# Kernel tuning notes

Hardware: AMD Instinct MI355X
Metric: run time of the kernel (lower is better)

Reference implementation:

```python
import jax, jax.numpy as jnp
import numpy as np

N_EX, N_KC, D, HID, NHEADS = 10000, 500, 128, 128, 2
B, S = 256, 500
ALPHA = 0.2
NEG = -9e15


def setup_inputs() -> dict:
    key = jax.random.key(0)
    ks = jax.random.split(key, 24)
    sc = 0.1
    inp = {
        "adj_exercise_kc": jax.random.randint(ks[0], (N_EX, N_KC), 0, 2, dtype=jnp.int32),
        "kc_data": jax.random.randint(ks[1], (B, S), 0, N_KC).astype(jnp.int64),
        "exercise_data": jax.random.randint(ks[2], (B, S), 0, N_EX + 1).astype(jnp.int64),
        "exercise_respond_data": jax.random.randint(ks[3], (B, S), 0, 2 * N_EX + 1).astype(jnp.int64),
        "target": jax.random.randint(ks[4], (B * (S - 1), 1), 0, 2).astype(jnp.float32),
        # learned parameters
        "ex_embed": jax.random.normal(ks[5], (N_EX, D)) * sc,
        "kc_embed": jax.random.normal(ks[6], (N_KC, D)) * sc,
        "W1": jax.random.normal(ks[7], (NHEADS, D, D)) * sc,        # per-head shared proj
        "a_att": jax.random.normal(ks[8], (NHEADS, 2 * D, 1)) * sc,  # attention vector
        "E": jax.random.normal(ks[9], (NHEADS, D, D)) * sc,
        "rd_w": jax.random.normal(ks[10], (NHEADS, D, 2 * D)) * sc,  # reduceDim (mode 3)
        "rd_b": jnp.zeros((NHEADS, D)),
        "w_ih": jax.random.normal(ks[11], (4 * HID, 2 * D)) * sc,
        "w_hh": jax.random.normal(ks[12], (4 * HID, HID)) * sc,
        "b_ih": jnp.zeros((4 * HID,)),
        "b_hh": jnp.zeros((4 * HID,)),
        "fc1_w": jax.random.normal(ks[13], (HID, D + HID)) * sc,
        "fc1_b": jnp.zeros((HID,)),
        "fc2_w": jax.random.normal(ks[14], (1, HID)) * sc,
        "fc2_b": jnp.zeros((1,)),
    }
    return inp


def _gat_head(ex_h, kc_h, adj, W1h, ah, Eh, rdw, rdb):
    # mode == 3 GAT head. a_input @ a decomposes: e[i,j] = LReLU(exWh[i].a1 + kcWh[j].a2)
    kc_Wh = kc_h @ W1h                                   # [Nkc, D]
    ex_Wh = ex_h @ W1h                                   # [Nex, D]
    e = jax.nn.leaky_relu(ex_Wh @ ah[:D] + (kc_Wh @ ah[D:]).T, ALPHA)  # [Nex, Nkc]
    att = jax.nn.softmax(jnp.where(adj > 0, e, NEG), axis=1)
    new_kc = att @ kc_Wh                                 # [Nex, D]
    ex_Eh = ex_h @ Eh
    emb = jnp.concatenate([new_kc, new_kc * ex_Eh], axis=1) @ rdw.T + rdb
    return jax.nn.elu(emb)                               # [Nex, D]


def _lstm(x, w_ih, w_hh, b_ih, b_hh):
    # single-layer torch LSTM, gate order i,f,g,o
    b = x.shape[0]
    xg = jnp.einsum('bsi,gi->sbg', x, w_ih) + b_ih + b_hh  # [S,B,4H]

    def step(carry, xt):
        h, c = carry
        g = xt + h @ w_hh.T
        i, f, gg, o = jnp.split(g, 4, axis=-1)
        c = jax.nn.sigmoid(f) * c + jax.nn.sigmoid(i) * jnp.tanh(gg)
        h = jax.nn.sigmoid(o) * jnp.tanh(c)
        return (h, c), h

    init = (jnp.zeros((b, HID), x.dtype), jnp.zeros((b, HID), x.dtype))
    _, hs = jax.lax.scan(step, init, xg)
    return jnp.swapaxes(hs, 0, 1)                        # [B,S,H]


def _forward(adj, exercise_data, respond_data, target,
             ex_embed, kc_embed, W1, a_att, E, rd_w, rd_b,
             w_ih, w_hh, b_ih, b_hh, fc1_w, fc1_b, fc2_w, fc2_b):
    heads = jax.vmap(_gat_head, in_axes=(None, None, None, 0, 0, 0, 0, 0))(
        ex_embed, kc_embed, adj, W1, a_att, E, rd_w, rd_b)   # [NH, Nex, D]
    # torch: cat(dim=1).view(Nex, D, NH).mean(2) -> interleaved reshape of the concat
    cat = jnp.swapaxes(heads, 0, 1).reshape(N_EX, NHEADS * D)
    exercise_embedding = cat.reshape(N_EX, D, NHEADS).mean(-1)  # [Nex, D]

    emb0 = jnp.concatenate([jnp.zeros((1, D), exercise_embedding.dtype), exercise_embedding], 0)
    assess = emb0[exercise_data]                          # [B,S,D]

    zeros = jnp.zeros_like(exercise_embedding)
    resp_emb = jnp.concatenate([
        jnp.concatenate([zeros, exercise_embedding], -1),
        jnp.concatenate([exercise_embedding, zeros], -1)], 0)  # [2Nex, 2D]
    resp0 = jnp.concatenate([jnp.zeros((1, 2 * D), resp_emb.dtype), resp_emb], 0)
    lstm_input = resp0[respond_data]                      # [B,S,2D]

    learn = _lstm(lstm_input, w_ih, w_hh, b_ih, b_hh)[:, :S - 1, :]  # [B,S-1,H]
    assess = assess[:, 1:, :]                             # [B,S-1,D]

    y = jax.nn.relu(jnp.concatenate([learn, assess], -1) @ fc1_w.T + fc1_b)
    pred = (y @ fc2_w.T + fc2_b).reshape(-1)              # [B*(S-1)]
    t = target.reshape(-1)                                # all targets >= 0 => mask all-true
    # BCE with logits, mean reduction
    loss = jnp.mean(jnp.maximum(pred, 0) - pred * t + jnp.log1p(jnp.exp(-jnp.abs(pred))))
    return loss, jax.nn.sigmoid(pred), t


def reference(adj_exercise_kc, kc_data, exercise_data, exercise_respond_data, target,
              ex_embed, kc_embed, W1, a_att, E, rd_w, rd_b,
              w_ih, w_hh, b_ih, b_hh, fc1_w, fc1_b, fc2_w, fc2_b):
    del kc_data  # unused by the original forward body
    return _forward(adj_exercise_kc, exercise_data, exercise_respond_data, target,
                    ex_embed, kc_embed, W1, a_att, E, rd_w, rd_b,
                    w_ih, w_hh, b_ih, b_hh, fc1_w, fc1_b, fc2_w, fc2_b)
```

## Files before the change

### kernel.cpp

```cpp
#include <hip/hip_runtime.h>
#include <math.h>

#define N_EX 10000
#define N_KC 500
#define D 128
#define HID 128
#define BB 256
#define SS 500
#define NROWS 127744

typedef float vf4 __attribute__((ext_vector_type(4)));
typedef _Float16 hf2 __attribute__((ext_vector_type(2)));
typedef _Float16 hf8 __attribute__((ext_vector_type(8)));
typedef float f32x4 __attribute__((ext_vector_type(4)));

__device__ __forceinline__ float sigm(float x) { return 1.f / (1.f + __expf(-x)); }
__device__ __forceinline__ float tanh_fast(float x) { return 1.f - 2.f / (1.f + __expf(2.f * x)); }

__device__ __forceinline__ hf2 u2h(unsigned v) { union { unsigned u; hf2 h; } x; x.u = v; return x.h; }

__device__ __forceinline__ float quad_sum(float x) {
    int a = __builtin_amdgcn_update_dpp(0, __float_as_int(x), 0xB1, 0xF, 0xF, true);
    x += __int_as_float(a);
    int b = __builtin_amdgcn_update_dpp(0, __float_as_int(x), 0x4E, 0xF, 0xF, true);
    x += __int_as_float(b);
    return x;
}

__global__ void k_precomp(const float* rd_w, const float* w_ih, const float* fc1_w,
                          const float* b_ih, const float* b_hh, const float* W1, const float* a_att,
                          const float* w_hh,
                          float* rd_wT, unsigned short* w_all16, unsigned short* fc1A16,
                          float* gb512, float* v1,
                          unsigned short* wlstm16, float* projC) {
    int idx = blockIdx.x * blockDim.x + threadIdx.x;
    int stride = gridDim.x * blockDim.x;
    const int N1 = 2 * 256 * 128;
    const int NW = 1152 * 128;
    const int NF = 128 * 128;
    const int NG = 512;
    const int N7 = 256;
    const int N8 = 65536;
    int total = N1 + NW + NF + NG + N7 + N8;
    for (int tt = idx; tt < total; tt += stride) {
        int u = tt;
        if (u < N1) {
            int h = u / (256 * 128); int rem = u % (256 * 128); int c = rem / 128; int dd = rem % 128;
            rd_wT[u] = rd_w[h * 128 * 256 + dd * 256 + c];
        } else if ((u -= N1) < NW) {
            int n = u >> 7, k = u & 127;
            float val;
            if (n < 512) {
                int c = n; val = w_ih[((c & 3) * 128 + (c >> 2)) * 256 + 128 + k];
            } else if (n < 1024) {
                int c = n - 512; val = w_ih[((c & 3) * 128 + (c >> 2)) * 256 + k];
            } else {
                int j = n - 1024; val = fc1_w[j * 256 + 128 + k];
            }
            ((_Float16*)w_all16)[u] = (_Float16)val;
        } else if ((u -= NW) < NF) {
            int j = u >> 7, k = u & 127;
            ((_Float16*)fc1A16)[u] = (_Float16)fc1_w[j * 256 + k];
        } else if ((u -= NF) < NG) {
            int c = u;
            float v = b_ih[(c & 3) * 128 + (c >> 2)] + b_hh[(c & 3) * 128 + (c >> 2)];
            gb512[c] = v;
            projC[c] = v;
        } else if ((u -= NG) < N7) {
            int h = u / 128, k = u % 128;
            const float* wr = W1 + h * 16384 + k * 128;
            const float* av = a_att + h * 256;
            float acc = 0.f;
            for (int d = 0; d < 128; ++d) acc += wr[d] * av[d];
            v1[u] = acc;
        } else {
            u -= N7;
            int x = u & 7;
            int t = (u >> 3) & 511;
            int i = u >> 12;
            int g = i >> 2, j = i & 3;
            int uu = t >> 2, q = t & 3;
            float val = w_hh[(g * 128 + uu) * 128 + q * 32 + j * 8 + x];
            ((_Float16*)wlstm16)[u] = (_Float16)val;
        }
    }
}

__global__ void k_kc(const float* kc_embed, const float* W1, const float* a_att,
                     float* kcWhT, float* s_kc) {
    int j = blockIdx.x, h = blockIdx.y, d = threadIdx.x;
    __shared__ float row[128];
    __shared__ float red[128];
    row[d] = kc_embed[j * 128 + d];
    __syncthreads();
    const float* w = W1 + h * 16384;
    float acc = 0.f;
    for (int k = 0; k < 128; ++k) acc += row[k] * w[k * 128 + d];
    kcWhT[((size_t)(h * 128 + d)) * 500 + j] = acc;
    red[d] = acc * a_att[h * 256 + 128 + d];
    __syncthreads();
    for (int s = 64; s > 0; s >>= 1) { if (d < s) red[d] += red[d + s]; __syncthreads(); }
    if (d == 0) s_kc[h * 500 + j] = red[0];
}

__global__ void k_sex(const float* ex_embed, const float* v1, float* s_ex) {
    int t = blockIdx.x * blockDim.x + threadIdx.x;
    if (t >= 2 * N_EX) return;
    int h = t / N_EX, i = t % N_EX;
    const float4* e4 = (const float4*)(ex_embed + (size_t)i * 128);
    const float4* v4 = (const float4*)(v1 + h * 128);
    float acc = 0.f;
    for (int k = 0; k < 32; ++k) {
        float4 a = e4[k], b = v4[k];
        acc += a.x * b.x + a.y * b.y + a.z * b.z + a.w * b.w;
    }
    s_ex[h * N_EX + i] = acc;
}

__global__ __launch_bounds__(256) void k_attnk(const int* adj, const float* s_ex, const float* s_kc,
                                               const float* kcWhT, float* new_kc) {
    int i0 = blockIdx.x * 8, t = threadIdx.x;
    __shared__ vf4 at4[2][1500];
    __shared__ float skc_l[2][500];
    float* at0 = (float*)at4[0];
    float* at1 = (float*)at4[1];
    for (int j = t; j < 1000; j += 256) ((float*)skc_l)[j] = s_kc[j];
    __syncthreads();
    {
        int lg = t >> 5, lane = t & 31;
        int i = i0 + lg;
        float sex0 = s_ex[i];
        float sex1 = s_ex[N_EX + i];
        const int* arow = adj + (size_t)i * 500;
        float lmax0 = -INFINITY, lmax1 = -INFINITY;
        for (int j = lane; j < 500; j += 32) {
            bool m = arow[j] > 0;
            float e0 = sex0 + skc_l[0][j];
            e0 = (e0 >= 0.f) ? e0 : 0.2f * e0;
            e0 = m ? e0 : -INFINITY;
            float e1 = sex1 + skc_l[1][j];
            e1 = (e1 >= 0.f) ? e1 : 0.2f * e1;
            e1 = m ? e1 : -INFINITY;
            at0[j * 12 + lg] = e0;
            at1[j * 12 + lg] = e1;
            lmax0 = fmaxf(lmax0, e0);
            lmax1 = fmaxf(lmax1, e1);
        }
#pragma unroll
        for (int m = 16; m > 0; m >>= 1) {
            lmax0 = fmaxf(lmax0, __shfl_xor(lmax0, m));
            lmax1 = fmaxf(lmax1, __shfl_xor(lmax1, m));
        }
        float lsum0 = 0.f, lsum1 = 0.f;
        for (int j = lane; j < 500; j += 32) {
            float w0 = __expf(at0[j * 12 + lg] - lmax0);
            float w1 = __expf(at1[j * 12 + lg] - lmax1);
            at0[j * 12 + lg] = w0;
            at1[j * 12 + lg] = w1;
            lsum0 += w0; lsum1 += w1;
        }
#pragma unroll
        for (int m = 16; m > 0; m >>= 1) {
            lsum0 += __shfl_xor(lsum0, m);
            lsum1 += __shfl_xor(lsum1, m);
        }
        float inv0 = 1.f / lsum0, inv1 = 1.f / lsum1;
        for (int j = lane; j < 500; j += 32) {
            at0[j * 12 + lg] *= inv0;
            at1[j * 12 + lg] *= inv1;
        }
    }
    __syncthreads();
    int d = t & 127, half = t >> 7;
    for (int h = 0; h < 2; ++h) {
        const float* at = (h == 0) ? at0 : at1;
        const float* kcwd = kcWhT + ((size_t)(h * 128 + d)) * 500;
        vf4 acc = {0.f, 0.f, 0.f, 0.f};
        for (int j4 = 0; j4 < 125; ++j4) {
            vf4 w = *(const vf4*)(kcwd + j4 * 4);
            vf4 a0 = *(const vf4*)(at + (j4 * 4 + 0) * 12 + half * 4);
            vf4 a1 = *(const vf4*)(at + (j4 * 4 + 1) * 12 + half * 4);
            vf4 a2 = *(const vf4*)(at + (j4 * 4 + 2) * 12 + half * 4);
            vf4 a3 = *(const vf4*)(at + (j4 * 4 + 3) * 12 + half * 4);
            acc += a0 * w.x + a1 * w.y + a2 * w.z + a3 * w.w;
        }
        new_kc[((size_t)h * N_EX + i0 + half * 4 + 0) * 128 + d] = acc.x;
        new_kc[((size_t)h * N_EX + i0 + half * 4 + 1) * 128 + d] = acc.y;
        new_kc[((size_t)h * N_EX + i0 + half * 4 + 2) * 128 + d] = acc.z;
        new_kc[((size_t)h * N_EX + i0 + half * 4 + 3) * 128 + d] = acc.w;
    }
}

__global__ __launch_bounds__(256) void k_gat2m(const float* new_kc, const float* ex_embed,
                                               const float* E, const float* rd_wT,
                                               const float* rd_b, _Float16* emb16) {
    int i0 = blockIdx.x * 8, t = threadIdx.x;
    int d = t & 127, half = t >> 7;
    __shared__ float exrT[128 * 8];
    __shared__ float nkT[2][128 * 8];
    __shared__ float prT[128 * 8];
    __shared__ float Hl[2][8 * 128];
    for (int idx = t; idx < 8 * 128; idx += 256) {
        int r = idx >> 7, k = idx & 127;
        exrT[k * 8 + r]   = ex_embed[(size_t)i0 * 128 + idx];
        nkT[0][k * 8 + r] = new_kc[((size_t)i0) * 128 + idx];
        nkT[1][k * 8 + r] = new_kc[((size_t)N_EX + i0) * 128 + idx];
    }
    __syncthreads();
    for (int h = 0; h < 2; ++h) {
        const float* Eh = E + h * 16384;
        const float* rt = rd_wT + h * 256 * 128;
        float rb = rd_b[h * 128 + d];
        vf4 acc2 = {0.f, 0.f, 0.f, 0.f};
        for (int k = 0; k < 128; ++k) {
            float ev = Eh[k * 128 + d];
            vf4 ex4 = *(const vf4*)(exrT + k * 8 + half * 4);
            acc2 += ex4 * ev;
        }
        {
            vf4 nk4 = *(const vf4*)(nkT[h] + d * 8 + half * 4);
            *(vf4*)(prT + d * 8 + half * 4) = nk4 * acc2;
        }
        __syncthreads();
        vf4 acc3 = {0.f, 0.f, 0.f, 0.f};
        for (int c = 0; c < 128; ++c) {
            float w = rt[c * 128 + d];
            vf4 nk4 = *(const vf4*)(nkT[h] + c * 8 + half * 4);
            acc3 += nk4 * w;
        }
        for (int c = 0; c < 128; ++c) {
            float w = rt[(128 + c) * 128 + d];
            vf4 pr4 = *(const vf4*)(prT + c * 8 + half * 4);
            acc3 += pr4 * w;
        }
#pragma unroll
        for (int r = 0; r < 4; ++r) {
            float v = ((r == 0) ? acc3.x : (r == 1) ? acc3.y : (r == 2) ? acc3.z : acc3.w) + rb;
            v = (v > 0.f) ? v : expm1f(v);
            Hl[h][(half * 4 + r) * 128 + d] = v;
        }
        __syncthreads();
    }
    for (int idx = t; idx < 8 * 128; idx += 256) {
        int r = idx >> 7, dd = idx & 127;
        int hs = dd >> 6;
        int c0 = (2 * dd) & 127, c1 = (2 * dd + 1) & 127;
        emb16[((size_t)i0 + r) * 128 + dd] =
            (_Float16)(0.5f * (Hl[hs][r * 128 + c0] + Hl[hs][r * 128 + c1]));
    }
}

__global__ __launch_bounds__(256) void k_projM(const unsigned short* __restrict__ emb16,
                                               const unsigned short* __restrict__ w_all16,
                                               const float* __restrict__ gb512,
                                               float* __restrict__ projC,
                                               float* __restrict__ assessP) {
    int mt = blockIdx.x, nt = blockIdx.y;
    int i0 = mt * 64, n0 = nt * 64;
    int t = threadIdx.x;
    __shared__ _Float16 Al[64 * 136];
    __shared__ _Float16 Bl[64 * 136];
    for (int idx = t; idx < 512; idx += 256) {
        int r = idx >> 3, sg = idx & 7;
        int gi = i0 + r; if (gi >= N_EX) gi = N_EX - 1;
        *(uint4*)(Al + r * 136 + sg * 8) = *(const uint4*)(emb16 + (size_t)gi * 128 + sg * 8);
    }
    for (int idx = t; idx < 512; idx += 256) {
        int r = idx >> 3, sg = idx & 7;
        *(uint4*)(Bl + r * 136 + sg * 8) = *(const uint4*)(w_all16 + (size_t)(n0 + r) * 128 + sg * 8);
    }
    __syncthreads();
    int w = t >> 6, l = t & 63, quad = l >> 4, lx = l & 15;
    const _Float16* ab = Al + ((w << 4) + lx) * 136 + (quad << 3);
    hf8 a0 = *(const hf8*)(ab);
    hf8 a1 = *(const hf8*)(ab + 32);
    hf8 a2 = *(const hf8*)(ab + 64);
    hf8 a3 = *(const hf8*)(ab + 96);
    f32x4 acc[4];
#pragma unroll
    for (int ct = 0; ct < 4; ++ct) {
        const _Float16* bb = Bl + ((ct << 4) + lx) * 136 + (quad << 3);
        f32x4 c = {0.f, 0.f, 0.f, 0.f};
        c = __builtin_amdgcn_mfma_f32_16x16x32_f16(a0, *(const hf8*)(bb),      c, 0, 0, 0);
        c = __builtin_amdgcn_mfma_f32_16x16x32_f16(a1, *(const hf8*)(bb + 32), c, 0, 0, 0);
        c = __builtin_amdgcn_mfma_f32_16x16x32_f16(a2, *(const hf8*)(bb + 64), c, 0, 0, 0);
        c = __builtin_amdgcn_mfma_f32_16x16x32_f16(a3, *(const hf8*)(bb + 96), c, 0, 0, 0);
        acc[ct] = c;
    }
    int rbase = i0 + (w << 4) + (quad << 2);
    if (nt < 16) {
        size_t rowbase = (nt < 8) ? 1 : (size_t)(1 + N_EX);
        int cc = n0 & 511;
#pragma unroll
        for (int ct = 0; ct < 4; ++ct) {
            int col = cc + (ct << 4) + lx;
            float gb = gb512[col];
#pragma unroll
            for (int reg = 0; reg < 4; ++reg) {
                int gi = rbase + reg;
                if (gi < N_EX) projC[(rowbase + gi) * 512 + col] = acc[ct][reg] + gb;
            }
        }
    } else {
        int cc = n0 - 1024;
#pragma unroll
        for (int ct = 0; ct < 4; ++ct) {
            int col = cc + (ct << 4) + lx;
#pragma unroll
            for (int reg = 0; reg < 4; ++reg) {
                int gi = rbase + reg;
                if (gi < N_EX) assessP[(size_t)gi * 128 + col] = acc[ct][reg];
            }
        }
    }
}

__global__ __launch_bounds__(512, 2) void k_lstm(const uint4* __restrict__ w16,
                                                 const float* __restrict__ projC,
                                                 const int* __restrict__ respond,
                                                 unsigned short* __restrict__ learn16) {
    int b = blockIdx.x, t = threadIdx.x;
    int u = t >> 2, q = t & 3;
    __shared__ uint4 hbuf4[2][18];
    __shared__ int rrow[500];
    uint4 w[16];
#pragma unroll
    for (int i = 0; i < 16; ++i) w[i] = w16[i * 512 + t];
    for (int s = t; s < 500; s += 512) rrow[s] = respond[b * 500 + s];
    if (t < 36) { uint4 z = {0u, 0u, 0u, 0u}; ((uint4*)hbuf4)[t] = z; }
    float c = 0.f;
    __syncthreads();
    vf4 xg_n = ((const vf4*)(projC + (size_t)rrow[0] * 512))[u];
    for (int s = 0; s < 500; ++s) {
        int par = s & 1;
        vf4 xg = xg_n;
        if (s < 499) xg_n = ((const vf4*)(projC + (size_t)rrow[s + 1] * 512))[u];
        const uint4* hsegp = (const uint4*)((const unsigned short*)hbuf4[par] + q * 32);
        uint4 h4[4];
#pragma unroll
        for (int j = 0; j < 4; ++j) h4[j] = hsegp[j];
        float p0 = 0.f, p1 = 0.f, p2 = 0.f, p3 = 0.f;
#pragma unroll
        for (int j = 0; j < 4; ++j) {
            hf2 ha = u2h(h4[j].x), hb = u2h(h4[j].y), hc = u2h(h4[j].z), hd = u2h(h4[j].w);
            uint4 w0 = w[j], w1 = w[4 + j], w2 = w[8 + j], w3 = w[12 + j];
            p0 = __builtin_amdgcn_fdot2(u2h(w0.x), ha, p0, false);
            p0 = __builtin_amdgcn_fdot2(u2h(w0.y), hb, p0, false);
            p0 = __builtin_amdgcn_fdot2(u2h(w0.z), hc, p0, false);
            p0 = __builtin_amdgcn_fdot2(u2h(w0.w), hd, p0, false);
            p1 = __builtin_amdgcn_fdot2(u2h(w1.x), ha, p1, false);
            p1 = __builtin_amdgcn_fdot2(u2h(w1.y), hb, p1, false);
            p1 = __builtin_amdgcn_fdot2(u2h(w1.z), hc, p1, false);
            p1 = __builtin_amdgcn_fdot2(u2h(w1.w), hd, p1, false);
            p2 = __builtin_amdgcn_fdot2(u2h(w2.x), ha, p2, false);
            p2 = __builtin_amdgcn_fdot2(u2h(w2.y), hb, p2, false);
            p2 = __builtin_amdgcn_fdot2(u2h(w2.z), hc, p2, false);
            p2 = __builtin_amdgcn_fdot2(u2h(w2.w), hd, p2, false);
            p3 = __builtin_amdgcn_fdot2(u2h(w3.x), ha, p3, false);
            p3 = __builtin_amdgcn_fdot2(u2h(w3.y), hb, p3, false);
            p3 = __builtin_amdgcn_fdot2(u2h(w3.z), hc, p3, false);
            p3 = __builtin_amdgcn_fdot2(u2h(w3.w), hd, p3, false);
        }
        float gi = quad_sum(p0) + xg.x;
        float gf = quad_sum(p1) + xg.y;
        float gG = quad_sum(p2) + xg.z;
        float go = quad_sum(p3) + xg.w;
        float ii = sigm(gi), ff = sigm(gf), tg = tanh_fast(gG), oo = sigm(go);
        c = ff * c + ii * tg;
        float hh = oo * tanh_fast(c);
        if (q == 0) {
            union { unsigned short us; _Float16 hf; } cv; cv.hf = (_Float16)hh;
            ((unsigned short*)hbuf4[par ^ 1])[u] = cv.us;
            if (s < 499) learn16[((size_t)b * 499 + s) * 128 + u] = cv.us;
        }
        __syncthreads();
    }
}

__global__ __launch_bounds__(256) void k_mlpM(const unsigned short* __restrict__ learn16,
                                              const unsigned short* __restrict__ fc1A16,
                                              const float* __restrict__ assessP,
                                              const float* __restrict__ fc1_b,
                                              const float* __restrict__ fc2_w,
                                              const float* __restrict__ fc2_b,
                                              const int* __restrict__ exercise_data,
                                              const float* __restrict__ target,
                                              float* __restrict__ out,
                                              float* __restrict__ loss_accum) {
    int tile = blockIdx.x;
    int row0 = tile * 64;
    int t = threadIdx.x;
    __shared__ _Float16 Al[64 * 136];
    __shared__ _Float16 Bl[128 * 136];
    __shared__ float red[4];
    for (int idx = t; idx < 512; idx += 256) {
        int r = idx >> 3, sg = idx & 7;
        *(uint4*)(Al + r * 136 + sg * 8) = *(const uint4*)(learn16 + ((size_t)row0 + r) * 128 + sg * 8);
    }
    for (int idx = t; idx < 1024; idx += 256) {
        int r = idx >> 3, sg = idx & 7;
        *(uint4*)(Bl + r * 136 + sg * 8) = *(const uint4*)(fc1A16 + r * 128 + sg * 8);
    }
    __syncthreads();
    int w = t >> 6, l = t & 63, quad = l >> 4, lx = l & 15;
    const _Float16* ab = Al + ((w << 4) + lx) * 136 + (quad << 3);
    hf8 a0 = *(const hf8*)(ab);
    hf8 a1 = *(const hf8*)(ab + 32);
    hf8 a2 = *(const hf8*)(ab + 64);
    hf8 a3 = *(const hf8*)(ab + 96);
    f32x4 acc[8];
#pragma unroll
    for (int ct = 0; ct < 8; ++ct) {
        const _Float16* bb = Bl + ((ct << 4) + lx) * 136 + (quad << 3);
        f32x4 c = {0.f, 0.f, 0.f, 0.f};
        c = __builtin_amdgcn_mfma_f32_16x16x32_f16(a0, *(const hf8*)(bb),      c, 0, 0, 0);
        c = __builtin_amdgcn_mfma_f32_16x16x32_f16(a1, *(const hf8*)(bb + 32), c, 0, 0, 0);
        c = __builtin_amdgcn_mfma_f32_16x16x32_f16(a2, *(const hf8*)(bb + 64), c, 0, 0, 0);
        c = __builtin_amdgcn_mfma_f32_16x16x32_f16(a3, *(const hf8*)(bb + 96), c, 0, 0, 0);
        acc[ct] = c;
    }
    int eidx[4];
#pragma unroll
    for (int reg = 0; reg < 4; ++reg) {
        int n = row0 + (w << 4) + (quad << 2) + reg;
        int b = n / 499, sidx = n - b * 499;
        eidx[reg] = exercise_data[b * 500 + sidx + 1];
    }
    float rs[4] = {0.f, 0.f, 0.f, 0.f};
#pragma unroll
    for (int ct = 0; ct < 8; ++ct) {
        int col = (ct << 4) + lx;
        float b1v = fc1_b[col], f2v = fc2_w[col];
#pragma unroll
        for (int reg = 0; reg < 4; ++reg) {
            float aP = (eidx[reg] > 0) ? assessP[(size_t)(eidx[reg] - 1) * 128 + col] : 0.f;
            float y = acc[ct][reg] + aP + b1v;
            y = y > 0.f ? y : 0.f;
            rs[reg] += y * f2v;
        }
    }
#pragma unroll
    for (int reg = 0; reg < 4; ++reg) {
        float s = rs[reg];
        s += __shfl_xor(s, 1); s += __shfl_xor(s, 2); s += __shfl_xor(s, 4); s += __shfl_xor(s, 8);
        rs[reg] = s;
    }
    float fb2 = fc2_b[0];
    float lloss = 0.f;
    if (lx == 0) {
#pragma unroll
        for (int reg = 0; reg < 4; ++reg) {
            int n = row0 + (w << 4) + (quad << 2) + reg;
            float p = rs[reg] + fb2;
            float tg = target[n];
            out[1 + n] = 1.f / (1.f + expf(-p));
            float ab2 = fabsf(p);
            lloss += fmaxf(p, 0.f) - p * tg + log1pf(expf(-ab2));
            out[1 + NROWS + n] = tg;
        }
    }
    lloss += __shfl_xor(lloss, 16);
    lloss += __shfl_xor(lloss, 32);
    if (l == 0) red[w] = lloss;
    __syncthreads();
    if (t == 0) atomicAdd(loss_accum, red[0] + red[1] + red[2] + red[3]);
}

__global__ void k_final(const float* loss_accum, float* out) {
    out[0] = loss_accum[0] * (1.f / (float)NROWS);
}

extern "C" void kernel_launch(void* const* d_in, const int* in_sizes, int n_in,
                              void* d_out, int out_size, void* d_ws, size_t ws_size,
                              hipStream_t stream) {
    const int* adj            = (const int*)d_in[0];
    const int* exercise_data  = (const int*)d_in[2];
    const int* respond        = (const int*)d_in[3];
    const float* target       = (const float*)d_in[4];
    const float* ex_embed     = (const float*)d_in[5];
    const float* kc_embed     = (const float*)d_in[6];
    const float* W1           = (const float*)d_in[7];
    const float* a_att        = (const float*)d_in[8];
    const float* E            = (const float*)d_in[9];
    const float* rd_w         = (const float*)d_in[10];
    const float* rd_b         = (const float*)d_in[11];
    const float* w_ih         = (const float*)d_in[12];
    const float* w_hh         = (const float*)d_in[13];
    const float* b_ih         = (const float*)d_in[14];
    const float* b_hh         = (const float*)d_in[15];
    const float* fc1_w        = (const float*)d_in[16];
    const float* fc1_b        = (const float*)d_in[17];
    const float* fc2_w        = (const float*)d_in[18];
    const float* fc2_b        = (const float*)d_in[19];
    float* out = (float*)d_out;

    float* ws = (float*)d_ws;
    size_t off = 0;
    auto alloc = [&](size_t n) { float* p = ws + off; off += (n + 3) & ~(size_t)3; return p; };
    float* kcWhT   = alloc(2 * 128 * 500);
    float* s_kc    = alloc(1000);
    float* v1      = alloc(256);
    float* s_ex    = alloc(2 * N_EX);
    float* rd_wT   = alloc(2 * 256 * 128);
    float* wlstm   = alloc(32768);
    float* w_all16 = alloc(1152 * 64);
    float* fc1A16  = alloc(8192);
    float* gb512   = alloc(512);
    float* emb16   = alloc((size_t)N_EX * 64);
    float* new_kc  = alloc((size_t)2 * N_EX * 128);
    float* projC   = alloc((size_t)(2 * N_EX + 1) * 512);
    float* assessP = alloc((size_t)N_EX * 128);
    float* learn16 = alloc((size_t)BB * 499 * 64);
    float* loss_accum = alloc(4);

    k_precomp<<<256, 256, 0, stream>>>(rd_w, w_ih, fc1_w, b_ih, b_hh, W1, a_att, w_hh,
                                       rd_wT, (unsigned short*)w_all16, (unsigned short*)fc1A16,
                                       gb512, v1, (unsigned short*)wlstm, projC);
    k_kc<<<dim3(500, 2), 128, 0, stream>>>(kc_embed, W1, a_att, kcWhT, s_kc);
    k_sex<<<79, 256, 0, stream>>>(ex_embed, v1, s_ex);
    k_attnk<<<N_EX / 8, 256, 0, stream>>>(adj, s_ex, s_kc, kcWhT, new_kc);
    k_gat2m<<<N_EX / 8, 256, 0, stream>>>(new_kc, ex_embed, E, rd_wT, rd_b, (_Float16*)emb16);
    k_projM<<<dim3(157, 18), 256, 0, stream>>>((const unsigned short*)emb16,
                                               (const unsigned short*)w_all16, gb512,
                                               projC, assessP);
    hipMemsetAsync(loss_accum, 0, sizeof(float), stream);
    k_lstm<<<BB, 512, 0, stream>>>((const uint4*)wlstm, projC, respond,
                                   (unsigned short*)learn16);
    k_mlpM<<<NROWS / 64, 256, 0, stream>>>((const unsigned short*)learn16,
                                           (const unsigned short*)fc1A16, assessP,
                                           fc1_b, fc2_w, fc2_b,
                                           exercise_data, target, out, loss_accum);
    k_final<<<1, 1, 0, stream>>>(loss_accum, out);
}
```

Measured before the change: 697.2 us.

## Batch 16 sequences per LSTM block with MFMA recurrence and fp16 gate projections

The LSTM recurrence moves from one batch row per block, using per-thread fdot2 dot products and DPP quad reductions, to 16 batch rows per block. Each wave now computes its gate tiles with 16x16x32 f16 MFMAs against a weight fragment layout precomputed in k_precomp. The precomputed input projections (projC) are stored as fp16 instead of fp32, which halves the per-step gather traffic and the write traffic in k_projM. The aim is to cut the per-step recurrent matmul cost and the memory traffic. In exchange only 16 blocks are launched, so most of the GPU sits idle, and fp16 storage of the gate pre-activations adds rounding error.

```diff
diff --git a/kernel.cpp b/kernel.cpp
--- a/kernel.cpp
+++ b/kernel.cpp
@@ -18,13 +18,8 @@
 __device__ __forceinline__ float tanh_fast(float x) { return 1.f - 2.f / (1.f + __expf(2.f * x)); }
 
 __device__ __forceinline__ hf2 u2h(unsigned v) { union { unsigned u; hf2 h; } x; x.u = v; return x.h; }
-
-__device__ __forceinline__ float quad_sum(float x) {
-    int a = __builtin_amdgcn_update_dpp(0, __float_as_int(x), 0xB1, 0xF, 0xF, true);
-    x += __int_as_float(a);
-    int b = __builtin_amdgcn_update_dpp(0, __float_as_int(x), 0x4E, 0xF, 0xF, true);
-    x += __int_as_float(b);
-    return x;
+__device__ __forceinline__ unsigned short f2us(float v) {
+    union { unsigned short us; _Float16 hf; } cv; cv.hf = (_Float16)v; return cv.us;
 }
 
 __global__ void k_precomp(const float* rd_w, const float* w_ih, const float* fc1_w,
@@ -32,7 +27,7 @@
                           const float* w_hh,
                           float* rd_wT, unsigned short* w_all16, unsigned short* fc1A16,
                           float* gb512, float* v1,
-                          unsigned short* wlstm16, float* projC) {
+                          unsigned short* wlstmA, unsigned short* projC16) {
     int idx = blockIdx.x * blockDim.x + threadIdx.x;
     int stride = gridDim.x * blockDim.x;
     const int N1 = 2 * 256 * 128;
@@ -65,7 +60,7 @@
             int c = u;
             float v = b_ih[(c & 3) * 128 + (c >> 2)] + b_hh[(c & 3) * 128 + (c >> 2)];
             gb512[c] = v;
-            projC[c] = v;
+            projC16[c] = f2us(v);
         } else if ((u -= NG) < N7) {
             int h = u / 128, k = u % 128;
             const float* wr = W1 + h * 16384 + k * 128;
@@ -75,13 +70,14 @@
             v1[u] = acc;
         } else {
             u -= N7;
-            int x = u & 7;
-            int t = (u >> 3) & 511;
-            int i = u >> 12;
-            int g = i >> 2, j = i & 3;
-            int uu = t >> 2, q = t & 3;
-            float val = w_hh[(g * 128 + uu) * 128 + q * 32 + j * 8 + x];
-            ((_Float16*)wlstm16)[u] = (_Float16)val;
+            int j = u & 7;
+            int lane = (u >> 3) & 63;
+            int frag = u >> 9;
+            int kc = frag & 3, mt = frag >> 2;
+            int m = mt * 16 + (lane & 15);
+            int k = kc * 32 + (lane >> 4) * 8 + j;
+            float val = w_hh[((m & 3) * 128 + (m >> 2)) * 128 + k];
+            ((_Float16*)wlstmA)[u] = (_Float16)val;
         }
     }
 }
@@ -253,7 +249,7 @@
 __global__ __launch_bounds__(256) void k_projM(const unsigned short* __restrict__ emb16,
                                                const unsigned short* __restrict__ w_all16,
                                                const float* __restrict__ gb512,
-                                               float* __restrict__ projC,
+                                               unsigned short* __restrict__ projC16,
                                                float* __restrict__ assessP) {
     int mt = blockIdx.x, nt = blockIdx.y;
     int i0 = mt * 64, n0 = nt * 64;
@@ -298,7 +294,7 @@
 #pragma unroll
             for (int reg = 0; reg < 4; ++reg) {
                 int gi = rbase + reg;
-                if (gi < N_EX) projC[(rowbase + gi) * 512 + col] = acc[ct][reg] + gb;
+                if (gi < N_EX) projC16[(rowbase + gi) * 512 + col] = f2us(acc[ct][reg] + gb);
             }
         }
     } else {
@@ -315,63 +311,76 @@
     }
 }
 
-__global__ __launch_bounds__(512, 2) void k_lstm(const uint4* __restrict__ w16,
-                                                 const float* __restrict__ projC,
+__global__ __launch_bounds__(512, 2) void k_lstm(const _Float16* __restrict__ wA,
+                                                 const unsigned short* __restrict__ projC16,
                                                  const int* __restrict__ respond,
                                                  unsigned short* __restrict__ learn16) {
-    int b = blockIdx.x, t = threadIdx.x;
-    int u = t >> 2, q = t & 3;
-    __shared__ uint4 hbuf4[2][18];
-    __shared__ int rrow[500];
-    uint4 w[16];
-#pragma unroll
-    for (int i = 0; i < 16; ++i) w[i] = w16[i * 512 + t];
-    for (int s = t; s < 500; s += 512) rrow[s] = respond[b * 500 + s];
-    if (t < 36) { uint4 z = {0u, 0u, 0u, 0u}; ((uint4*)hbuf4)[t] = z; }
-    float c = 0.f;
-    __syncthreads();
-    vf4 xg_n = ((const vf4*)(projC + (size_t)rrow[0] * 512))[u];
+    int blk = blockIdx.x, t = threadIdx.x;
+    int w = t >> 6, lane = t & 63, quad = lane >> 4, n = lane & 15;
+    __shared__ _Float16 HB[2][16 * 136];
+    __shared__ int rrow[16 * 500];
+    for (int idx = t; idx < 8000; idx += 512) {
+        int nn = idx / 500, ss = idx - nn * 500;
+        rrow[nn * 500 + ss] = respond[((size_t)blk * 16 + nn) * 500 + ss];
+    }
+    for (int idx = t; idx < 2 * 16 * 136; idx += 512) ((_Float16*)HB)[idx] = (_Float16)0.f;
+    hf8 a[4][4];
+#pragma unroll
+    for (int tt = 0; tt < 4; ++tt)
+#pragma unroll
+        for (int kc = 0; kc < 4; ++kc)
+            a[tt][kc] = *(const hf8*)(wA + ((((4 * w + tt) * 4 + kc) * 64) + lane) * 8);
+    float cst[4] = {0.f, 0.f, 0.f, 0.f};
+    __syncthreads();
+    uint2 xgp[4];
+    {
+        int r0 = rrow[n * 500];
+        const unsigned short* pr = projC16 + (size_t)r0 * 512;
+#pragma unroll
+        for (int tt = 0; tt < 4; ++tt) {
+            int u = 16 * w + 4 * tt + quad;
+            xgp[tt] = *(const uint2*)(pr + u * 4);
+        }
+    }
     for (int s = 0; s < 500; ++s) {
         int par = s & 1;
-        vf4 xg = xg_n;
-        if (s < 499) xg_n = ((const vf4*)(projC + (size_t)rrow[s + 1] * 512))[u];
-        const uint4* hsegp = (const uint4*)((const unsigned short*)hbuf4[par] + q * 32);
-        uint4 h4[4];
-#pragma unroll
-        for (int j = 0; j < 4; ++j) h4[j] = hsegp[j];
-        float p0 = 0.f, p1 = 0.f, p2 = 0.f, p3 = 0.f;
-#pragma unroll
-        for (int j = 0; j < 4; ++j) {
-            hf2 ha = u2h(h4[j].x), hb = u2h(h4[j].y), hc = u2h(h4[j].z), hd = u2h(h4[j].w);
-            uint4 w0 = w[j], w1 = w[4 + j], w2 = w[8 + j], w3 = w[12 + j];
-            p0 = __builtin_amdgcn_fdot2(u2h(w0.x), ha, p0, false);
-            p0 = __builtin_amdgcn_fdot2(u2h(w0.y), hb, p0, false);
-            p0 = __builtin_amdgcn_fdot2(u2h(w0.z), hc, p0, false);
-            p0 = __builtin_amdgcn_fdot2(u2h(w0.w), hd, p0, false);
-            p1 = __builtin_amdgcn_fdot2(u2h(w1.x), ha, p1, false);
-            p1 = __builtin_amdgcn_fdot2(u2h(w1.y), hb, p1, false);
-            p1 = __builtin_amdgcn_fdot2(u2h(w1.z), hc, p1, false);
-            p1 = __builtin_amdgcn_fdot2(u2h(w1.w), hd, p1, false);
-            p2 = __builtin_amdgcn_fdot2(u2h(w2.x), ha, p2, false);
-            p2 = __builtin_amdgcn_fdot2(u2h(w2.y), hb, p2, false);
-            p2 = __builtin_amdgcn_fdot2(u2h(w2.z), hc, p2, false);
-            p2 = __builtin_amdgcn_fdot2(u2h(w2.w), hd, p2, false);
-            p3 = __builtin_amdgcn_fdot2(u2h(w3.x), ha, p3, false);
-            p3 = __builtin_amdgcn_fdot2(u2h(w3.y), hb, p3, false);
-            p3 = __builtin_amdgcn_fdot2(u2h(w3.z), hc, p3, false);
-            p3 = __builtin_amdgcn_fdot2(u2h(w3.w), hd, p3, false);
-        }
-        float gi = quad_sum(p0) + xg.x;
-        float gf = quad_sum(p1) + xg.y;
-        float gG = quad_sum(p2) + xg.z;
-        float go = quad_sum(p3) + xg.w;
-        float ii = sigm(gi), ff = sigm(gf), tg = tanh_fast(gG), oo = sigm(go);
-        c = ff * c + ii * tg;
-        float hh = oo * tanh_fast(c);
-        if (q == 0) {
-            union { unsigned short us; _Float16 hf; } cv; cv.hf = (_Float16)hh;
-            ((unsigned short*)hbuf4[par ^ 1])[u] = cv.us;
-            if (s < 499) learn16[((size_t)b * 499 + s) * 128 + u] = cv.us;
+        if (s > 0) {
+            int nn = t >> 5, uu = (t & 31) * 4;
+            unsigned long long v = *(const unsigned long long*)(&HB[par][nn * 136 + uu]);
+            *(unsigned long long*)(learn16 + (((size_t)(blk * 16 + nn)) * 499 + (s - 1)) * 128 + uu) = v;
+        }
+        uint2 xg[4];
+#pragma unroll
+        for (int tt = 0; tt < 4; ++tt) xg[tt] = xgp[tt];
+        if (s < 499) {
+            int rn = rrow[n * 500 + s + 1];
+            const unsigned short* pr = projC16 + (size_t)rn * 512;
+#pragma unroll
+            for (int tt = 0; tt < 4; ++tt) {
+                int u = 16 * w + 4 * tt + quad;
+                xgp[tt] = *(const uint2*)(pr + u * 4);
+            }
+        }
+        hf8 b[4];
+#pragma unroll
+        for (int kc = 0; kc < 4; ++kc)
+            b[kc] = *(const hf8*)(&HB[par][n * 136 + kc * 32 + quad * 8]);
+#pragma unroll
+        for (int tt = 0; tt < 4; ++tt) {
+            f32x4 c4 = {0.f, 0.f, 0.f, 0.f};
+#pragma unroll
+            for (int kc = 0; kc < 4; ++kc)
+                c4 = __builtin_amdgcn_mfma_f32_16x16x32_f16(a[tt][kc], b[kc], c4, 0, 0, 0);
+            hf2 x01 = u2h(xg[tt].x), x23 = u2h(xg[tt].y);
+            float gi = c4[0] + (float)x01.x;
+            float gf = c4[1] + (float)x01.y;
+            float gg = c4[2] + (float)x23.x;
+            float go = c4[3] + (float)x23.y;
+            float ii = sigm(gi), ff = sigm(gf), tg = tanh_fast(gg), oo = sigm(go);
+            cst[tt] = ff * cst[tt] + ii * tg;
+            float hh = oo * tanh_fast(cst[tt]);
+            int u = 16 * w + 4 * tt + quad;
+            HB[par ^ 1][n * 136 + u] = (_Float16)hh;
         }
         __syncthreads();
     }
@@ -502,30 +511,31 @@
     float* v1      = alloc(256);
     float* s_ex    = alloc(2 * N_EX);
     float* rd_wT   = alloc(2 * 256 * 128);
-    float* wlstm   = alloc(32768);
+    float* wlstmA  = alloc(32768);
     float* w_all16 = alloc(1152 * 64);
     float* fc1A16  = alloc(8192);
     float* gb512   = alloc(512);
     float* emb16   = alloc((size_t)N_EX * 64);
     float* new_kc  = alloc((size_t)2 * N_EX * 128);
-    float* projC   = alloc((size_t)(2 * N_EX + 1) * 512);
+    float* projC16 = alloc(((size_t)(2 * N_EX + 1) * 512) / 2);
     float* assessP = alloc((size_t)N_EX * 128);
     float* learn16 = alloc((size_t)BB * 499 * 64);
     float* loss_accum = alloc(4);
 
     k_precomp<<<256, 256, 0, stream>>>(rd_w, w_ih, fc1_w, b_ih, b_hh, W1, a_att, w_hh,
                                        rd_wT, (unsigned short*)w_all16, (unsigned short*)fc1A16,
-                                       gb512, v1, (unsigned short*)wlstm, projC);
+                                       gb512, v1, (unsigned short*)wlstmA,
+                                       (unsigned short*)projC16);
     k_kc<<<dim3(500, 2), 128, 0, stream>>>(kc_embed, W1, a_att, kcWhT, s_kc);
     k_sex<<<79, 256, 0, stream>>>(ex_embed, v1, s_ex);
     k_attnk<<<N_EX / 8, 256, 0, stream>>>(adj, s_ex, s_kc, kcWhT, new_kc);
     k_gat2m<<<N_EX / 8, 256, 0, stream>>>(new_kc, ex_embed, E, rd_wT, rd_b, (_Float16*)emb16);
     k_projM<<<dim3(157, 18), 256, 0, stream>>>((const unsigned short*)emb16,
                                                (const unsigned short*)w_all16, gb512,
-                                               projC, assessP);
+                                               (unsigned short*)projC16, assessP);
     hipMemsetAsync(loss_accum, 0, sizeof(float), stream);
-    k_lstm<<<BB, 512, 0, stream>>>((const uint4*)wlstm, projC, respond,
-                                   (unsigned short*)learn16);
+    k_lstm<<<16, 512, 0, stream>>>((const _Float16*)wlstmA, (const unsigned short*)projC16,
+                                   respond, (unsigned short*)learn16);
     k_mlpM<<<NROWS / 64, 256, 0, stream>>>((const unsigned short*)learn16,
                                            (const unsigned short*)fc1A16, assessP,
                                            fc1_b, fc2_w, fc2_b,
```

After: 1.162 ms. 1.67x slower.
